# Optimization experiments

Measured on AMD Instinct MI355X. Metric: run time of the kernel, lower is better.

The kernel has to match this reference:

```python
import jax, jax.numpy as jnp
import numpy as np

B, C, H, W = 64, 512, 32, 32   # batch, channels (=in_dim=model_dim), spatial
N, A = 1, 16                   # n_routers (forced to 1 by the view/matmul shape algebra), num_adapters
EPS = 1e-5                     # torch BatchNorm2d / LayerNorm default eps
INIT_SCALE = 0.02              # config.router_init_scale


def setup_inputs() -> dict:
    key = jax.random.key(0)
    k1, k2 = jax.random.split(key)
    x = jax.random.normal(k1, (B, C, H, W), dtype=jnp.float32)
    router_weights = jax.random.normal(k2, (N, C, A), dtype=jnp.float32) * INIT_SCALE
    router_bias = jnp.zeros((N, A), dtype=jnp.float32)
    bn_gamma = jnp.ones((N, C), dtype=jnp.float32)          # BatchNorm2d weight per router
    bn_beta = jnp.zeros((N, C), dtype=jnp.float32)          # BatchNorm2d bias per router
    ln_gamma = jnp.ones((N, C), dtype=jnp.float32) * INIT_SCALE  # LayerNorm weight (init'd to router_init_scale)
    ln_beta = jnp.zeros((N, C), dtype=jnp.float32)          # LayerNorm bias per router
    return dict(x=x, router_weights=router_weights, router_bias=router_bias,
                bn_gamma=bn_gamma, bn_beta=bn_beta, ln_gamma=ln_gamma, ln_beta=ln_beta)


def reference(x, router_weights, router_bias, bn_gamma, bn_beta, ln_gamma, ln_beta):
    # --- per-router BatchNorm2d (training-mode batch stats over N,H,W) + spatial mean pool ---
    mu = jnp.mean(x, axis=(0, 2, 3))                         # [C]
    var = jnp.var(x, axis=(0, 2, 3))                         # biased, as torch uses for normalization
    xn = (x - mu[None, :, None, None]) * jax.lax.rsqrt(var + EPS)[None, :, None, None]

    def bn_pool(g, b):  # g,b: [C] -> pooled [B,C]
        return jnp.mean(xn * g[None, :, None, None] + b[None, :, None, None], axis=(2, 3))

    new_x = jax.vmap(bn_pool)(bn_gamma, bn_beta)             # [N,B,C]

    # --- normalize_router_weights: LayerNorm over in_dim of router_weights[i].T ---
    wt = jnp.swapaxes(router_weights, 1, 2)                  # [N,A,C]
    m = jnp.mean(wt, axis=-1, keepdims=True)
    v = jnp.var(wt, axis=-1, keepdims=True)
    wn = (wt - m) * jax.lax.rsqrt(v + EPS) * ln_gamma[:, None, :] + ln_beta[:, None, :]
    wn = jnp.swapaxes(wn, 1, 2)                              # [N,C,A]

    # --- routing matmul + bias + softmax (equiv. to view(B,-1) @ W for N=1) ---
    adapter_logits = jnp.einsum('nbc,nca->nba', new_x, wn) + router_bias[:, None, :]  # [N,B,A]
    adapter_probs = jax.nn.softmax(adapter_logits, axis=-1)
    return new_x, adapter_logits, adapter_probs
```

## Files before the change

### kernel.cpp

```cpp
#include <hip/hip_runtime.h>

#define B_DIM 64
#define C_DIM 512
#define A_DIM 16
#define HW    1024
#define EPS   1e-5f

__global__ __launch_bounds__(256) void reduce_rows(const float* __restrict__ x,
                                                   float* __restrict__ s1,
                                                   float* __restrict__ sq) {
    const int bc = blockIdx.x;
    const float4* p = reinterpret_cast<const float4*>(x + (size_t)bc * HW);
    float4 v = p[threadIdx.x];
    float s = v.x + v.y + v.z + v.w;
    float q = v.x * v.x + v.y * v.y + v.z * v.z + v.w * v.w;
#pragma unroll
    for (int off = 32; off > 0; off >>= 1) {
        s += __shfl_down(s, off);
        q += __shfl_down(q, off);
    }
    __shared__ float ls[4], lq[4];
    const int wid = threadIdx.x >> 6;
    const int lane = threadIdx.x & 63;
    if (lane == 0) { ls[wid] = s; lq[wid] = q; }
    __syncthreads();
    if (threadIdx.x == 0) {
        s = ls[0] + ls[1] + ls[2] + ls[3];
        q = lq[0] + lq[1] + lq[2] + lq[3];
        const int b = bc >> 9;
        const int c = bc & (C_DIM - 1);
        s1[c * B_DIM + b] = s;
        sq[c * B_DIM + b] = q;
    }
}

__global__ __launch_bounds__(64) void stats_newx_ln(
    const float* __restrict__ s1, const float* __restrict__ sq,
    const float* __restrict__ bn_g, const float* __restrict__ bn_b,
    const float* __restrict__ rw, const float* __restrict__ ln_g,
    const float* __restrict__ ln_b,
    float* __restrict__ newx, float* __restrict__ wn_t) {
    const int lane = threadIdx.x;
    if (blockIdx.x < C_DIM) {
        const int c = blockIdx.x;
        const float s = s1[c * B_DIM + lane];
        const float q = sq[c * B_DIM + lane];
        float ts = s, tq = q;
#pragma unroll
        for (int off = 32; off > 0; off >>= 1) {
            ts += __shfl_down(ts, off);
            tq += __shfl_down(tq, off);
        }
        const float mu  = __shfl(ts, 0) * (1.0f / 65536.0f);
        const float var = __shfl(tq, 0) * (1.0f / 65536.0f) - mu * mu;
        const float r   = rsqrtf(var + EPS);
        const float nx  = bn_g[c] * (s * (1.0f / 1024.0f) - mu) * r + bn_b[c];
        newx[lane * C_DIM + c] = nx;
    } else {
        const int a = blockIdx.x - C_DIM;
        float wv[8];
        float s = 0.f, q = 0.f;
#pragma unroll
        for (int j = 0; j < 8; j++) {
            const int c = j * 64 + lane;
            wv[j] = rw[c * A_DIM + a];
            s += wv[j];
            q += wv[j] * wv[j];
        }
#pragma unroll
        for (int off = 32; off > 0; off >>= 1) {
            s += __shfl_down(s, off);
            q += __shfl_down(q, off);
        }
        const float m = __shfl(s, 0) * (1.0f / 512.0f);
        const float v = __shfl(q, 0) * (1.0f / 512.0f) - m * m;
        const float r = rsqrtf(v + EPS);
#pragma unroll
        for (int j = 0; j < 8; j++) {
            const int c = j * 64 + lane;
            wn_t[c * A_DIM + a] = (wv[j] - m) * r * ln_g[c] + ln_b[c];
        }
    }
}

__global__ __launch_bounds__(64) void matmul_softmax(
    const float* __restrict__ newx, const float* __restrict__ wn_t,
    const float* __restrict__ rbias,
    float* __restrict__ logits, float* __restrict__ probs) {
    const int b = blockIdx.x;
    const int lane = threadIdx.x;
    const int a = lane & 15;
    const int chunk = lane >> 4;
    const float* xr = newx + b * C_DIM + chunk * 128;
    const float* wr = wn_t + (chunk * 128) * A_DIM + a;
    float acc = 0.f;
#pragma unroll 8
    for (int i = 0; i < 128; i++) {
        acc += xr[i] * wr[i * A_DIM];
    }
    acc += __shfl_xor(acc, 16);
    acc += __shfl_xor(acc, 32);
    const float logit = acc + rbias[a];
    float mx = logit;
#pragma unroll
    for (int m = 1; m < 16; m <<= 1) mx = fmaxf(mx, __shfl_xor(mx, m));
    const float e = expf(logit - mx);
    float se = e;
#pragma unroll
    for (int m = 1; m < 16; m <<= 1) se += __shfl_xor(se, m);
    const float prob = e / se;
    if (lane < 16) {
        logits[b * A_DIM + lane] = logit;
        probs[b * A_DIM + lane] = prob;
    }
}

extern "C" void kernel_launch(void* const* d_in, const int* in_sizes, int n_in,
                              void* d_out, int out_size, void* d_ws, size_t ws_size,
                              hipStream_t stream) {
    const float* x     = (const float*)d_in[0];
    const float* rw    = (const float*)d_in[1];
    const float* rbias = (const float*)d_in[2];
    const float* bn_g  = (const float*)d_in[3];
    const float* bn_b  = (const float*)d_in[4];
    const float* ln_g  = (const float*)d_in[5];
    const float* ln_b  = (const float*)d_in[6];

    float* out    = (float*)d_out;
    float* newx   = out;
    float* logits = out + B_DIM * C_DIM;
    float* probs  = logits + B_DIM * A_DIM;

    float* s1   = (float*)d_ws;
    float* sq   = s1 + B_DIM * C_DIM;
    float* wn_t = sq + B_DIM * C_DIM;

    reduce_rows<<<B_DIM * C_DIM, 256, 0, stream>>>(x, s1, sq);
    stats_newx_ln<<<C_DIM + A_DIM, 64, 0, stream>>>(s1, sq, bn_g, bn_b, rw,
                                                    ln_g, ln_b, newx, wn_t);
    matmul_softmax<<<B_DIM, 64, 0, stream>>>(newx, wn_t, rbias, logits, probs);
}
```

Measured before the change: 201.7 us.

## Reduce two rows per wave without LDS and pack sum/sumsq as float2

The row-reduction kernel now gives each 64-lane wave two full 1024-element rows, loading eight float4 per lane, so each block covers eight rows and the grid shrinks eightfold. This removes the shared-memory exchange and __syncthreads and gives each lane more loads in flight. The sum and sum-of-squares partials are stored interleaved as float2, so the stats kernel reads them with one load instead of two. Fewer blocks could reduce occupancy or tail balance on a memory-bound 128 MB read.

```diff
diff --git a/kernel.cpp b/kernel.cpp
--- a/kernel.cpp
+++ b/kernel.cpp
@@ -7,35 +7,52 @@
 #define EPS   1e-5f
 
 __global__ __launch_bounds__(256) void reduce_rows(const float* __restrict__ x,
-                                                   float* __restrict__ s1,
-                                                   float* __restrict__ sq) {
-    const int bc = blockIdx.x;
-    const float4* p = reinterpret_cast<const float4*>(x + (size_t)bc * HW);
-    float4 v = p[threadIdx.x];
-    float s = v.x + v.y + v.z + v.w;
-    float q = v.x * v.x + v.y * v.y + v.z * v.z + v.w * v.w;
+                                                   float2* __restrict__ sums) {
+    const int wave = threadIdx.x >> 6;
+    const int lane = threadIdx.x & 63;
+    const int rowA = blockIdx.x * 8 + wave * 2;
+    const int rowB = rowA + 1;
+    const float4* pA = reinterpret_cast<const float4*>(x) + (size_t)rowA * 256;
+    const float4* pB = reinterpret_cast<const float4*>(x) + (size_t)rowB * 256;
+    const float4 a0 = pA[lane];
+    const float4 a1 = pA[lane + 64];
+    const float4 a2 = pA[lane + 128];
+    const float4 a3 = pA[lane + 192];
+    const float4 b0 = pB[lane];
+    const float4 b1 = pB[lane + 64];
+    const float4 b2 = pB[lane + 128];
+    const float4 b3 = pB[lane + 192];
+
+    float sA = (a0.x + a0.y + a0.z + a0.w) + (a1.x + a1.y + a1.z + a1.w)
+             + (a2.x + a2.y + a2.z + a2.w) + (a3.x + a3.y + a3.z + a3.w);
+    float qA = (a0.x * a0.x + a0.y * a0.y + a0.z * a0.z + a0.w * a0.w)
+             + (a1.x * a1.x + a1.y * a1.y + a1.z * a1.z + a1.w * a1.w)
+             + (a2.x * a2.x + a2.y * a2.y + a2.z * a2.z + a2.w * a2.w)
+             + (a3.x * a3.x + a3.y * a3.y + a3.z * a3.z + a3.w * a3.w);
+    float sB = (b0.x + b0.y + b0.z + b0.w) + (b1.x + b1.y + b1.z + b1.w)
+             + (b2.x + b2.y + b2.z + b2.w) + (b3.x + b3.y + b3.z + b3.w);
+    float qB = (b0.x * b0.x + b0.y * b0.y + b0.z * b0.z + b0.w * b0.w)
+             + (b1.x * b1.x + b1.y * b1.y + b1.z * b1.z + b1.w * b1.w)
+             + (b2.x * b2.x + b2.y * b2.y + b2.z * b2.z + b2.w * b2.w)
+             + (b3.x * b3.x + b3.y * b3.y + b3.z * b3.z + b3.w * b3.w);
+
 #pragma unroll
     for (int off = 32; off > 0; off >>= 1) {
-        s += __shfl_down(s, off);
-        q += __shfl_down(q, off);
+        sA += __shfl_down(sA, off);
+        qA += __shfl_down(qA, off);
+        sB += __shfl_down(sB, off);
+        qB += __shfl_down(qB, off);
     }
-    __shared__ float ls[4], lq[4];
-    const int wid = threadIdx.x >> 6;
-    const int lane = threadIdx.x & 63;
-    if (lane == 0) { ls[wid] = s; lq[wid] = q; }
-    __syncthreads();
-    if (threadIdx.x == 0) {
-        s = ls[0] + ls[1] + ls[2] + ls[3];
-        q = lq[0] + lq[1] + lq[2] + lq[3];
-        const int b = bc >> 9;
-        const int c = bc & (C_DIM - 1);
-        s1[c * B_DIM + b] = s;
-        sq[c * B_DIM + b] = q;
+    if (lane == 0) {
+        int b = rowA >> 9, c = rowA & (C_DIM - 1);
+        sums[c * B_DIM + b] = make_float2(sA, qA);
+        b = rowB >> 9;  c = rowB & (C_DIM - 1);
+        sums[c * B_DIM + b] = make_float2(sB, qB);
     }
 }
 
 __global__ __launch_bounds__(64) void stats_newx_ln(
-    const float* __restrict__ s1, const float* __restrict__ sq,
+    const float2* __restrict__ sums,
     const float* __restrict__ bn_g, const float* __restrict__ bn_b,
     const float* __restrict__ rw, const float* __restrict__ ln_g,
     const float* __restrict__ ln_b,
@@ -43,9 +60,8 @@
     const int lane = threadIdx.x;
     if (blockIdx.x < C_DIM) {
         const int c = blockIdx.x;
-        const float s = s1[c * B_DIM + lane];
-        const float q = sq[c * B_DIM + lane];
-        float ts = s, tq = q;
+        const float2 t = sums[c * B_DIM + lane];
+        float ts = t.x, tq = t.y;
 #pragma unroll
         for (int off = 32; off > 0; off >>= 1) {
             ts += __shfl_down(ts, off);
@@ -54,7 +70,7 @@
         const float mu  = __shfl(ts, 0) * (1.0f / 65536.0f);
         const float var = __shfl(tq, 0) * (1.0f / 65536.0f) - mu * mu;
         const float r   = rsqrtf(var + EPS);
-        const float nx  = bn_g[c] * (s * (1.0f / 1024.0f) - mu) * r + bn_b[c];
+        const float nx  = bn_g[c] * (t.x * (1.0f / 1024.0f) - mu) * r + bn_b[c];
         newx[lane * C_DIM + c] = nx;
     } else {
         const int a = blockIdx.x - C_DIM;
@@ -131,12 +147,11 @@
     float* logits = out + B_DIM * C_DIM;
     float* probs  = logits + B_DIM * A_DIM;
 
-    float* s1   = (float*)d_ws;
-    float* sq   = s1 + B_DIM * C_DIM;
-    float* wn_t = sq + B_DIM * C_DIM;
+    float2* sums = (float2*)d_ws;
+    float*  wn_t = (float*)(sums + B_DIM * C_DIM);
 
-    reduce_rows<<<B_DIM * C_DIM, 256, 0, stream>>>(x, s1, sq);
-    stats_newx_ln<<<C_DIM + A_DIM, 64, 0, stream>>>(s1, sq, bn_g, bn_b, rw,
+    reduce_rows<<<(B_DIM * C_DIM) / 8, 256, 0, stream>>>(x, sums);
+    stats_newx_ln<<<C_DIM + A_DIM, 64, 0, stream>>>(sums, bn_g, bn_b, rw,
                                                     ln_g, ln_b, newx, wn_t);
     matmul_softmax<<<B_DIM, 64, 0, stream>>>(newx, wn_t, rbias, logits, probs);
 }
```

New measurement: 206.1 us. 2.2% more time.
